# Kernel optimization log

Measured on AMD Instinct MI355X. Metric: run time of the kernel, lower is better.

The kernel has to match this reference:

```python
import jax, jax.numpy as jnp
import numpy as np

N, D, H, DH, E = 4096, 256, 4, 64, 131072  # nodes, embed dim, heads, head dim, edges
ALPHA = 0.2  # LeakyReLU negative slope
NEG = -9.0e15  # mask fill value from the torch code (-9000000000000000.0)


def setup_inputs() -> dict:
    key = jax.random.key(0)
    ks = jax.random.split(key, 10)
    x = jax.random.normal(ks[0], (N, D), dtype=jnp.float32)
    edge_index = jax.random.randint(ks[1], (2, E), 0, N, dtype=jnp.int32)
    edge_vals = jax.random.uniform(ks[2], (E,), dtype=jnp.float32)
    # EdgeWeightAttention MLP: Linear(2D -> D), ReLU, Linear(D -> 1)
    W1 = jax.random.normal(ks[3], (2 * D, D), dtype=jnp.float32) * (1.0 / np.sqrt(2 * D))
    b1 = jnp.zeros((D,), dtype=jnp.float32)
    W2 = jax.random.normal(ks[4], (D, 1), dtype=jnp.float32) * (1.0 / np.sqrt(D))
    b2 = jnp.zeros((1,), dtype=jnp.float32)
    # Per-head GAT params (stacked over heads): W [H, D, DH], a_src/a_dst [H, DH]
    gain = 1.414
    W = jax.random.normal(ks[5], (H, D, DH), dtype=jnp.float32) * (gain * np.sqrt(2.0 / (D + DH)))
    a_src = jax.random.normal(ks[6], (H, DH), dtype=jnp.float32) * (gain * np.sqrt(2.0 / (1 + DH)))
    a_dst = jax.random.normal(ks[7], (H, DH), dtype=jnp.float32) * (gain * np.sqrt(2.0 / (1 + DH)))
    return {"x": x, "edge_vals": edge_vals, "W1": W1, "b1": b1, "W2": W2, "b2": b2,
            "W": W, "a_src": a_src, "a_dst": a_dst, "edge_index": edge_index}


def reference(x, edge_vals, W1, b1, W2, b2, W, a_src, a_dst, edge_index):
    n = x.shape[0]
    row, col = edge_index[0], edge_index[1]
    # --- EdgeWeightAttention: gather endpoint features, tiny MLP + sigmoid, rescale edge values ---
    ef = jnp.concatenate([x[row], x[col]], axis=1)                       # [E, 2D]
    aw = jax.nn.sigmoid(jax.nn.relu(ef @ W1 + b1) @ W2 + b2)[:, 0]       # [E]
    new_vals = edge_vals * aw                                            # [E]
    # Densify reweighted sparse adj (values are positive -> used only as mask adj>0 in GAT)
    adj = jnp.zeros((n, n), dtype=x.dtype).at[row, col].set(new_vals)    # [N, N]
    # --- Multi-head GAT, vectorized over heads ---
    h = jnp.einsum('nd,hde->hne', x, W)                                  # [H, N, DH]
    esrc = jnp.einsum('hne,he->hn', h, a_src)                            # [H, N]
    edst = jnp.einsum('hne,he->hn', h, a_dst)                            # [H, N]
    e = jax.nn.leaky_relu(esrc[:, :, None] + edst[:, None, :], ALPHA)    # [H, N, N]
    e = jnp.where(adj[None, :, :] > 0, e, jnp.asarray(NEG, x.dtype))
    attn = jax.nn.softmax(e, axis=-1)                                    # [H, N, N]
    out = jnp.einsum('hij,hje->hie', attn, h)                            # [H, N, DH]
    return jnp.transpose(out, (1, 0, 2)).reshape(n, H * DH)              # [N, D]
```

## Files before the change

### kernel.cpp

```cpp
#include <hip/hip_runtime.h>
#include <hip/hip_bf16.h>

#define NN    4096
#define DD    256
#define HH    4
#define DHH   64
#define EDGES 131072
#define CAP   128
#define RPB   2
#define LRELU_ALPHA 0.2f

typedef __hip_bfloat16 bf16;
typedef __attribute__((ext_vector_type(8))) short short8v;
typedef __attribute__((ext_vector_type(4))) float f32x4;


__device__ __forceinline__ float bf_lo(unsigned int u) { return __uint_as_float(u << 16); }
__device__ __forceinline__ float bf_hi(unsigned int u) { return __uint_as_float(u & 0xffff0000u); }

__device__ __forceinline__ unsigned short f2bf_rne(float f) {
    unsigned int u = __float_as_uint(f);
    return (unsigned short)((u + 0x7fffu + ((u >> 16) & 1u)) >> 16);
}
__device__ __forceinline__ float bf2f(unsigned short s) {
    return __uint_as_float(((unsigned int)s) << 16);
}

__global__ __launch_bounds__(1024) void hproj_edges_kernel(
    const float* __restrict__ x, const float* __restrict__ W,
    const float* __restrict__ a_src, const float* __restrict__ a_dst,
    const int* __restrict__ ei, const float* __restrict__ ev,
    bf16* __restrict__ hb, float* __restrict__ esrc, float* __restrict__ edst,
    unsigned int* __restrict__ bmg)
{
    __shared__ unsigned short wlhi[2048 * 10];
    __shared__ unsigned short wllo[2048 * 10];
    __shared__ float pvs[16][16];
    __shared__ float pvd[16][16];

    const int t   = threadIdx.x;
    const int blk = blockIdx.x;
    const int h   = blk & 3;
    const int i0  = (blk >> 2) * 64;

    if (t < 512) {
        const int   e  = blk * 512 + t;
        const float vv = ev[e];
        const int   er = ei[e];
        const int   ec = ei[EDGES + e];
        if (vv > 0.f)
            atomicOr(&bmg[er * (NN / 32) + (ec >> 5)], 1u << (ec & 31));
    }

    {
        const float4* Ws = (const float4*)(W + (size_t)h * (DD * DHH));
        #pragma unroll
        for (int j = 0; j < 4; ++j) {
            const int fi = t + j * 1024;
            const float4 f = Ws[fi];
            const float v[4] = {f.x, f.y, f.z, f.w};
            #pragma unroll
            for (int c = 0; c < 4; ++c) {
                const int lin = fi * 4 + c;
                const int d = lin >> 6, dh = lin & 63;
                const int rec = (((dh >> 4) * 8 + (d >> 5)) << 6)
                              + ((d >> 3) & 3) * 16 + (dh & 15);
                const int off = rec * 10 + (d & 7);
                const unsigned short hi = f2bf_rne(v[c]);
                wlhi[off] = hi;
                wllo[off] = f2bf_rne(v[c] - bf2f(hi));
            }
        }
    }
    __syncthreads();

    const int wv   = t >> 6;
    const int m    = wv >> 2;
    const int q    = wv & 3;
    const int lane = t & 63;
    const int mrow = lane & 15;
    const int kgrp = lane >> 4;

    const float* xp = x + (size_t)(i0 + m * 16 + mrow) * DD + 8 * kgrp;
    const unsigned int* hi32 = (const unsigned int*)wlhi;
    const unsigned int* lo32 = (const unsigned int*)wllo;

    f32x4 acc = (f32x4){0.f, 0.f, 0.f, 0.f};

    #pragma unroll
    for (int ks = 0; ks < 8; ++ks) {
        const float4 u0 = *(const float4*)(xp + ks * 32);
        const float4 u1 = *(const float4*)(xp + ks * 32 + 4);
        const float v[8] = {u0.x, u0.y, u0.z, u0.w, u1.x, u1.y, u1.z, u1.w};
        short8v ah, al;
        #pragma unroll
        for (int e = 0; e < 8; ++e) {
            const unsigned short hi = f2bf_rne(v[e]);
            ah[e] = (short)hi;
            al[e] = (short)f2bf_rne(v[e] - bf2f(hi));
        }
        const int rb = ((q * 8 + ks) * 64 + lane) * 5;
        union { unsigned int u[4]; short8v s; } bh, bl;
        #pragma unroll
        for (int k = 0; k < 4; ++k) {
            bh.u[k] = hi32[rb + k];
            bl.u[k] = lo32[rb + k];
        }
        acc = __builtin_amdgcn_mfma_f32_16x16x32_bf16(ah, bh.s, acc, 0, 0, 0);
        acc = __builtin_amdgcn_mfma_f32_16x16x32_bf16(ah, bl.s, acc, 0, 0, 0);
        acc = __builtin_amdgcn_mfma_f32_16x16x32_bf16(al, bh.s, acc, 0, 0, 0);
    }

    {
        const int col = h * 64 + q * 16 + mrow;
        #pragma unroll
        for (int reg = 0; reg < 4; ++reg) {
            const int row = i0 + m * 16 + 4 * kgrp + reg;
            hb[(size_t)row * (HH * DHH) + col] = __float2bfloat16(acc[reg]);
        }
    }

    {
        const float as = a_src[h * DHH + q * 16 + mrow];
        const float ad = a_dst[h * DHH + q * 16 + mrow];
        float vs[4], vd[4];
        #pragma unroll
        for (int reg = 0; reg < 4; ++reg) {
            vs[reg] = acc[reg] * as;
            vd[reg] = acc[reg] * ad;
        }
        #pragma unroll
        for (int reg = 0; reg < 4; ++reg) {
            #pragma unroll
            for (int off = 1; off < 16; off <<= 1) {
                vs[reg] += __shfl_xor(vs[reg], off, 64);
                vd[reg] += __shfl_xor(vd[reg], off, 64);
            }
        }
        if (mrow == 0) {
            #pragma unroll
            for (int reg = 0; reg < 4; ++reg) {
                pvs[wv][4 * kgrp + reg] = vs[reg];
                pvd[wv][4 * kgrp + reg] = vd[reg];
            }
        }
    }
    __syncthreads();

    if (q == 0 && lane < 16) {
        float s = 0.f, d = 0.f;
        #pragma unroll
        for (int qq = 0; qq < 4; ++qq) {
            s += pvs[m * 4 + qq][lane];
            d += pvd[m * 4 + qq][lane];
        }
        const int row = i0 + m * 16 + lane;
        esrc[row * HH + h] = s;
        edst[row * HH + h] = d;
    }
}

__global__ __launch_bounds__(128) void attn_kernel(
    const unsigned int* __restrict__ bmg, const bf16* __restrict__ hb,
    const float* __restrict__ esrc, const float* __restrict__ edst,
    float* __restrict__ out)
{
    __shared__ int nbr[RPB][CAP];
    __shared__ __align__(16) float wts[RPB][CAP][HH];

    const int t = threadIdx.x;
    const int r = t >> 6, lane = t & 63;
    const int i = blockIdx.x * RPB + r;

    const uint2 wp = *(const uint2*)(bmg + (size_t)i * (NN / 32) + 2 * lane);
    const int c = __popc(wp.x) + __popc(wp.y);
    int inc = c;
    #pragma unroll
    for (int off = 1; off < 64; off <<= 1) {
        const int nn = __shfl_up(inc, off, 64);
        if (lane >= off) inc += nn;
    }
    int p = inc - c;
    const int deg = min(__shfl(inc, 63, 64), CAP);
    unsigned int w = wp.x;
    while (w) { const int b = __ffs(w) - 1; w &= w - 1; if (p < CAP) nbr[r][p] = (lane << 6) + b; ++p; }
    w = wp.y;
    while (w) { const int b = __ffs(w) - 1; w &= w - 1; if (p < CAP) nbr[r][p] = (lane << 6) + 32 + b; ++p; }
    __syncthreads();

    const int head = lane >> 4;
    float4 acc = make_float4(0.f, 0.f, 0.f, 0.f);
    float4 sm  = make_float4(0.f, 0.f, 0.f, 0.f);

    if (deg > 0) {
        const float4 es4 = *(const float4*)(esrc + (size_t)i * HH);
        float4 mx = make_float4(-INFINITY, -INFINITY, -INFINITY, -INFINITY);
        for (int k = lane; k < deg; k += 64) {
            const float4 ed = *(const float4*)(edst + (size_t)nbr[r][k] * HH);
            float4 e4;
            e4.x = es4.x + ed.x; e4.x = e4.x > 0.f ? e4.x : LRELU_ALPHA * e4.x;
            e4.y = es4.y + ed.y; e4.y = e4.y > 0.f ? e4.y : LRELU_ALPHA * e4.y;
            e4.z = es4.z + ed.z; e4.z = e4.z > 0.f ? e4.z : LRELU_ALPHA * e4.z;
            e4.w = es4.w + ed.w; e4.w = e4.w > 0.f ? e4.w : LRELU_ALPHA * e4.w;
            *(float4*)&wts[r][k][0] = e4;
            mx.x = fmaxf(mx.x, e4.x); mx.y = fmaxf(mx.y, e4.y);
            mx.z = fmaxf(mx.z, e4.z); mx.w = fmaxf(mx.w, e4.w);
        }
        #pragma unroll
        for (int off = 32; off; off >>= 1) {
            mx.x = fmaxf(mx.x, __shfl_xor(mx.x, off, 64));
            mx.y = fmaxf(mx.y, __shfl_xor(mx.y, off, 64));
            mx.z = fmaxf(mx.z, __shfl_xor(mx.z, off, 64));
            mx.w = fmaxf(mx.w, __shfl_xor(mx.w, off, 64));
        }
        for (int k = lane; k < deg; k += 64) {
            float4 e4 = *(const float4*)&wts[r][k][0];
            e4.x = expf(e4.x - mx.x); e4.y = expf(e4.y - mx.y);
            e4.z = expf(e4.z - mx.z); e4.w = expf(e4.w - mx.w);
            *(float4*)&wts[r][k][0] = e4;
            sm.x += e4.x; sm.y += e4.y; sm.z += e4.z; sm.w += e4.w;
        }
        #pragma unroll
        for (int off = 32; off; off >>= 1) {
            sm.x += __shfl_xor(sm.x, off, 64);
            sm.y += __shfl_xor(sm.y, off, 64);
            sm.z += __shfl_xor(sm.z, off, 64);
            sm.w += __shfl_xor(sm.w, off, 64);
        }
    }
    __syncthreads();

    float inv;
    if (deg == 0) {
        const uint2* hp = (const uint2*)hb + lane;
        for (int j = 0; j < NN; ++j) {
            const uint2 u = hp[(size_t)j * 64];
            acc.x += bf_lo(u.x); acc.y += bf_hi(u.x);
            acc.z += bf_lo(u.y); acc.w += bf_hi(u.y);
        }
        inv = 1.f / NN;
    } else {
        const uint2* hp = (const uint2*)hb;
        int k = 0;
        for (; k + 3 < deg; k += 4) {
            const int j0 = nbr[r][k],     j1 = nbr[r][k + 1];
            const int j2 = nbr[r][k + 2], j3 = nbr[r][k + 3];
            const uint2 u0 = hp[(size_t)j0 * 64 + lane];
            const uint2 u1 = hp[(size_t)j1 * 64 + lane];
            const uint2 u2 = hp[(size_t)j2 * 64 + lane];
            const uint2 u3 = hp[(size_t)j3 * 64 + lane];
            const float w0 = wts[r][k][head],     w1 = wts[r][k + 1][head];
            const float w2 = wts[r][k + 2][head], w3 = wts[r][k + 3][head];
            acc.x = fmaf(w0, bf_lo(u0.x), acc.x); acc.y = fmaf(w0, bf_hi(u0.x), acc.y);
            acc.z = fmaf(w0, bf_lo(u0.y), acc.z); acc.w = fmaf(w0, bf_hi(u0.y), acc.w);
            acc.x = fmaf(w1, bf_lo(u1.x), acc.x); acc.y = fmaf(w1, bf_hi(u1.x), acc.y);
            acc.z = fmaf(w1, bf_lo(u1.y), acc.z); acc.w = fmaf(w1, bf_hi(u1.y), acc.w);
            acc.x = fmaf(w2, bf_lo(u2.x), acc.x); acc.y = fmaf(w2, bf_hi(u2.x), acc.y);
            acc.z = fmaf(w2, bf_lo(u2.y), acc.z); acc.w = fmaf(w2, bf_hi(u2.y), acc.w);
            acc.x = fmaf(w3, bf_lo(u3.x), acc.x); acc.y = fmaf(w3, bf_hi(u3.x), acc.y);
            acc.z = fmaf(w3, bf_lo(u3.y), acc.z); acc.w = fmaf(w3, bf_hi(u3.y), acc.w);
        }
        for (; k < deg; ++k) {
            const uint2 u = hp[(size_t)nbr[r][k] * 64 + lane];
            const float wk = wts[r][k][head];
            acc.x = fmaf(wk, bf_lo(u.x), acc.x); acc.y = fmaf(wk, bf_hi(u.x), acc.y);
            acc.z = fmaf(wk, bf_lo(u.y), acc.z); acc.w = fmaf(wk, bf_hi(u.y), acc.w);
        }
        const float s = head == 0 ? sm.x : head == 1 ? sm.y : head == 2 ? sm.z : sm.w;
        inv = 1.f / s;
    }

    float4 o;
    o.x = acc.x * inv; o.y = acc.y * inv; o.z = acc.z * inv; o.w = acc.w * inv;
    *(float4*)(out + (size_t)i * (HH * DHH) + 4 * lane) = o;
}

extern "C" void kernel_launch(void* const* d_in, const int* in_sizes, int n_in,
                              void* d_out, int out_size, void* d_ws, size_t ws_size,
                              hipStream_t stream)
{
    const float* x     = (const float*)d_in[0];
    const float* ev    = (const float*)d_in[1];
    const float* W     = (const float*)d_in[6];
    const float* a_src = (const float*)d_in[7];
    const float* a_dst = (const float*)d_in[8];
    const int*   ei    = (const int*)d_in[9];
    float* out = (float*)d_out;

    char* ws = (char*)d_ws;
    bf16*  hb    = (bf16*)ws;
    float* esrc  = (float*)(ws + 2097152);
    float* edst  = (float*)(ws + 2162688);
    unsigned int* bmg = (unsigned int*)(ws + 2228224);

    hipMemsetAsync(bmg, 0, NN * (NN / 32) * sizeof(unsigned int), stream);
    hproj_edges_kernel<<<256, 1024, 0, stream>>>(x, W, a_src, a_dst, ei, ev,
                                                 hb, esrc, edst, bmg);
    attn_kernel<<<NN / RPB, 128, 0, stream>>>(bmg, hb, esrc, edst, out);
}
```

Measured before the change: 102.9 us.

## Fuse memset, projection and attention into one cooperative kernel with grid syncs

Replaces the memset plus two kernel launches with a single cooperative kernel of 256 blocks x 1024 threads. The blocks zero the adjacency bitmap themselves, do the projection and edge scatter, then run the attention phase with 16 rows per block, separated by grid-wide syncs. Shared memory is a union of the two phases' layouts. This removes launch overhead and inter-kernel gaps, but attention now runs on only 256 large blocks instead of 2048 small ones, and grid.sync adds its own cost.

```diff
diff --git a/kernel.cpp b/kernel.cpp
--- a/kernel.cpp
+++ b/kernel.cpp
@@ -1,5 +1,8 @@
 #include <hip/hip_runtime.h>
 #include <hip/hip_bf16.h>
+#include <hip/hip_cooperative_groups.h>
+
+namespace cg = cooperative_groups;
 
 #define NN    4096
 #define DD    256
@@ -7,7 +10,6 @@
 #define DHH   64
 #define EDGES 131072
 #define CAP   128
-#define RPB   2
 #define LRELU_ALPHA 0.2f
 
 typedef __hip_bfloat16 bf16;
@@ -26,253 +28,262 @@
     return __uint_as_float(((unsigned int)s) << 16);
 }
 
-__global__ __launch_bounds__(1024) void hproj_edges_kernel(
-    const float* __restrict__ x, const float* __restrict__ W,
-    const float* __restrict__ a_src, const float* __restrict__ a_dst,
-    const int* __restrict__ ei, const float* __restrict__ ev,
+struct Phase1LDS {
+    unsigned short wlhi[2048 * 10];
+    unsigned short wllo[2048 * 10];
+    float pvs[16][16];
+    float pvd[16][16];
+};
+struct Phase2LDS {
+    int   nbr[16][CAP];
+    float wts[16][CAP][HH];
+};
+union FusedLDS { Phase1LDS p1; Phase2LDS p2; };
+
+__global__ __launch_bounds__(1024, 4) void fused_kernel(
+    const float* __restrict__ x, const float* __restrict__ ev,
+    const float* __restrict__ W, const float* __restrict__ a_src,
+    const float* __restrict__ a_dst, const int* __restrict__ ei,
     bf16* __restrict__ hb, float* __restrict__ esrc, float* __restrict__ edst,
-    unsigned int* __restrict__ bmg)
+    unsigned int* __restrict__ bmg, float* __restrict__ out)
 {
-    __shared__ unsigned short wlhi[2048 * 10];
-    __shared__ unsigned short wllo[2048 * 10];
-    __shared__ float pvs[16][16];
-    __shared__ float pvd[16][16];
+    __shared__ FusedLDS sh;
+    cg::grid_group grid = cg::this_grid();
 
     const int t   = threadIdx.x;
     const int blk = blockIdx.x;
-    const int h   = blk & 3;
-    const int i0  = (blk >> 2) * 64;
-
-    if (t < 512) {
-        const int   e  = blk * 512 + t;
-        const float vv = ev[e];
-        const int   er = ei[e];
-        const int   ec = ei[EDGES + e];
-        if (vv > 0.f)
-            atomicOr(&bmg[er * (NN / 32) + (ec >> 5)], 1u << (ec & 31));
+
+    ((uint2*)bmg)[blk * 1024 + t] = make_uint2(0u, 0u);
+    grid.sync();
+
+    {
+        const int h  = blk & 3;
+        const int i0 = (blk >> 2) * 64;
+
+        if (t < 512) {
+            const int   e  = blk * 512 + t;
+            const float vv = ev[e];
+            const int   er = ei[e];
+            const int   ec = ei[EDGES + e];
+            if (vv > 0.f)
+                atomicOr(&bmg[er * (NN / 32) + (ec >> 5)], 1u << (ec & 31));
+        }
+
+        {
+            const float4* Ws = (const float4*)(W + (size_t)h * (DD * DHH));
+            #pragma unroll
+            for (int j = 0; j < 4; ++j) {
+                const int fi = t + j * 1024;
+                const float4 f = Ws[fi];
+                const float v[4] = {f.x, f.y, f.z, f.w};
+                #pragma unroll
+                for (int c = 0; c < 4; ++c) {
+                    const int lin = fi * 4 + c;
+                    const int d = lin >> 6, dh = lin & 63;
+                    const int rec = (((dh >> 4) * 8 + (d >> 5)) << 6)
+                                  + ((d >> 3) & 3) * 16 + (dh & 15);
+                    const int off = rec * 10 + (d & 7);
+                    const unsigned short hi = f2bf_rne(v[c]);
+                    sh.p1.wlhi[off] = hi;
+                    sh.p1.wllo[off] = f2bf_rne(v[c] - bf2f(hi));
+                }
+            }
+        }
+        __syncthreads();
+
+        const int wv   = t >> 6;
+        const int m    = wv >> 2;
+        const int q    = wv & 3;
+        const int lane = t & 63;
+        const int mrow = lane & 15;
+        const int kgrp = lane >> 4;
+
+        const float* xp = x + (size_t)(i0 + m * 16 + mrow) * DD + 8 * kgrp;
+        const unsigned int* hi32 = (const unsigned int*)sh.p1.wlhi;
+        const unsigned int* lo32 = (const unsigned int*)sh.p1.wllo;
+
+        f32x4 acc = (f32x4){0.f, 0.f, 0.f, 0.f};
+
+        #pragma unroll
+        for (int ks = 0; ks < 8; ++ks) {
+            const float4 u0 = *(const float4*)(xp + ks * 32);
+            const float4 u1 = *(const float4*)(xp + ks * 32 + 4);
+            const float v[8] = {u0.x, u0.y, u0.z, u0.w, u1.x, u1.y, u1.z, u1.w};
+            short8v ah, al;
+            #pragma unroll
+            for (int e = 0; e < 8; ++e) {
+                const unsigned short hi = f2bf_rne(v[e]);
+                ah[e] = (short)hi;
+                al[e] = (short)f2bf_rne(v[e] - bf2f(hi));
+            }
+            const int rb = ((q * 8 + ks) * 64 + lane) * 5;
+            union { unsigned int u[4]; short8v s; } bh, bl;
+            #pragma unroll
+            for (int k = 0; k < 4; ++k) {
+                bh.u[k] = hi32[rb + k];
+                bl.u[k] = lo32[rb + k];
+            }
+            acc = __builtin_amdgcn_mfma_f32_16x16x32_bf16(ah, bh.s, acc, 0, 0, 0);
+            acc = __builtin_amdgcn_mfma_f32_16x16x32_bf16(ah, bl.s, acc, 0, 0, 0);
+            acc = __builtin_amdgcn_mfma_f32_16x16x32_bf16(al, bh.s, acc, 0, 0, 0);
+        }
+
+        {
+            const int col = h * 64 + q * 16 + mrow;
+            #pragma unroll
+            for (int reg = 0; reg < 4; ++reg) {
+                const int row = i0 + m * 16 + 4 * kgrp + reg;
+                hb[(size_t)row * (HH * DHH) + col] = __float2bfloat16(acc[reg]);
+            }
+        }
+
+        {
+            const float as = a_src[h * DHH + q * 16 + mrow];
+            const float ad = a_dst[h * DHH + q * 16 + mrow];
+            float vs[4], vd[4];
+            #pragma unroll
+            for (int reg = 0; reg < 4; ++reg) {
+                vs[reg] = acc[reg] * as;
+                vd[reg] = acc[reg] * ad;
+            }
+            #pragma unroll
+            for (int reg = 0; reg < 4; ++reg) {
+                #pragma unroll
+                for (int off = 1; off < 16; off <<= 1) {
+                    vs[reg] += __shfl_xor(vs[reg], off, 64);
+                    vd[reg] += __shfl_xor(vd[reg], off, 64);
+                }
+            }
+            if (mrow == 0) {
+                #pragma unroll
+                for (int reg = 0; reg < 4; ++reg) {
+                    sh.p1.pvs[wv][4 * kgrp + reg] = vs[reg];
+                    sh.p1.pvd[wv][4 * kgrp + reg] = vd[reg];
+                }
+            }
+        }
+        __syncthreads();
+
+        if (q == 0 && lane < 16) {
+            float s = 0.f, d = 0.f;
+            #pragma unroll
+            for (int qq = 0; qq < 4; ++qq) {
+                s += sh.p1.pvs[m * 4 + qq][lane];
+                d += sh.p1.pvd[m * 4 + qq][lane];
+            }
+            const int row = i0 + m * 16 + lane;
+            esrc[row * HH + h] = s;
+            edst[row * HH + h] = d;
+        }
     }
+    grid.sync();
 
     {
-        const float4* Ws = (const float4*)(W + (size_t)h * (DD * DHH));
+        const int w = t >> 6, lane = t & 63;
+        const int i = blk * 16 + w;
+
+        const uint2 wp = *(const uint2*)(bmg + (size_t)i * (NN / 32) + 2 * lane);
+        const int c = __popc(wp.x) + __popc(wp.y);
+        int inc = c;
         #pragma unroll
-        for (int j = 0; j < 4; ++j) {
-            const int fi = t + j * 1024;
-            const float4 f = Ws[fi];
-            const float v[4] = {f.x, f.y, f.z, f.w};
-            #pragma unroll
-            for (int c = 0; c < 4; ++c) {
-                const int lin = fi * 4 + c;
-                const int d = lin >> 6, dh = lin & 63;
-                const int rec = (((dh >> 4) * 8 + (d >> 5)) << 6)
-                              + ((d >> 3) & 3) * 16 + (dh & 15);
-                const int off = rec * 10 + (d & 7);
-                const unsigned short hi = f2bf_rne(v[c]);
-                wlhi[off] = hi;
-                wllo[off] = f2bf_rne(v[c] - bf2f(hi));
-            }
-        }
+        for (int off = 1; off < 64; off <<= 1) {
+            const int nn = __shfl_up(inc, off, 64);
+            if (lane >= off) inc += nn;
+        }
+        int p = inc - c;
+        const int deg = min(__shfl(inc, 63, 64), CAP);
+        unsigned int bw = wp.x;
+        while (bw) { const int b = __ffs(bw) - 1; bw &= bw - 1; if (p < CAP) sh.p2.nbr[w][p] = (lane << 6) + b; ++p; }
+        bw = wp.y;
+        while (bw) { const int b = __ffs(bw) - 1; bw &= bw - 1; if (p < CAP) sh.p2.nbr[w][p] = (lane << 6) + 32 + b; ++p; }
+        __syncthreads();
+
+        const int head = lane >> 4;
+        float4 acc = make_float4(0.f, 0.f, 0.f, 0.f);
+        float4 sm  = make_float4(0.f, 0.f, 0.f, 0.f);
+
+        if (deg > 0) {
+            const float4 es4 = *(const float4*)(esrc + (size_t)i * HH);
+            float4 mx = make_float4(-INFINITY, -INFINITY, -INFINITY, -INFINITY);
+            for (int k = lane; k < deg; k += 64) {
+                const float4 ed = *(const float4*)(edst + (size_t)sh.p2.nbr[w][k] * HH);
+                float4 e4;
+                e4.x = es4.x + ed.x; e4.x = e4.x > 0.f ? e4.x : LRELU_ALPHA * e4.x;
+                e4.y = es4.y + ed.y; e4.y = e4.y > 0.f ? e4.y : LRELU_ALPHA * e4.y;
+                e4.z = es4.z + ed.z; e4.z = e4.z > 0.f ? e4.z : LRELU_ALPHA * e4.z;
+                e4.w = es4.w + ed.w; e4.w = e4.w > 0.f ? e4.w : LRELU_ALPHA * e4.w;
+                *(float4*)&sh.p2.wts[w][k][0] = e4;
+                mx.x = fmaxf(mx.x, e4.x); mx.y = fmaxf(mx.y, e4.y);
+                mx.z = fmaxf(mx.z, e4.z); mx.w = fmaxf(mx.w, e4.w);
+            }
+            #pragma unroll
+            for (int off = 32; off; off >>= 1) {
+                mx.x = fmaxf(mx.x, __shfl_xor(mx.x, off, 64));
+                mx.y = fmaxf(mx.y, __shfl_xor(mx.y, off, 64));
+                mx.z = fmaxf(mx.z, __shfl_xor(mx.z, off, 64));
+                mx.w = fmaxf(mx.w, __shfl_xor(mx.w, off, 64));
+            }
+            for (int k = lane; k < deg; k += 64) {
+                float4 e4 = *(const float4*)&sh.p2.wts[w][k][0];
+                e4.x = expf(e4.x - mx.x); e4.y = expf(e4.y - mx.y);
+                e4.z = expf(e4.z - mx.z); e4.w = expf(e4.w - mx.w);
+                *(float4*)&sh.p2.wts[w][k][0] = e4;
+                sm.x += e4.x; sm.y += e4.y; sm.z += e4.z; sm.w += e4.w;
+            }
+            #pragma unroll
+            for (int off = 32; off; off >>= 1) {
+                sm.x += __shfl_xor(sm.x, off, 64);
+                sm.y += __shfl_xor(sm.y, off, 64);
+                sm.z += __shfl_xor(sm.z, off, 64);
+                sm.w += __shfl_xor(sm.w, off, 64);
+            }
+        }
+        __syncthreads();
+
+        float inv;
+        if (deg == 0) {
+            const uint2* hp = (const uint2*)hb + lane;
+            for (int j = 0; j < NN; ++j) {
+                const uint2 u = hp[(size_t)j * 64];
+                acc.x += bf_lo(u.x); acc.y += bf_hi(u.x);
+                acc.z += bf_lo(u.y); acc.w += bf_hi(u.y);
+            }
+            inv = 1.f / NN;
+        } else {
+            const uint2* hp = (const uint2*)hb;
+            int k = 0;
+            for (; k + 3 < deg; k += 4) {
+                const int j0 = sh.p2.nbr[w][k],     j1 = sh.p2.nbr[w][k + 1];
+                const int j2 = sh.p2.nbr[w][k + 2], j3 = sh.p2.nbr[w][k + 3];
+                const uint2 u0 = hp[(size_t)j0 * 64 + lane];
+                const uint2 u1 = hp[(size_t)j1 * 64 + lane];
+                const uint2 u2 = hp[(size_t)j2 * 64 + lane];
+                const uint2 u3 = hp[(size_t)j3 * 64 + lane];
+                const float w0 = sh.p2.wts[w][k][head],     w1 = sh.p2.wts[w][k + 1][head];
+                const float w2 = sh.p2.wts[w][k + 2][head], w3 = sh.p2.wts[w][k + 3][head];
+                acc.x = fmaf(w0, bf_lo(u0.x), acc.x); acc.y = fmaf(w0, bf_hi(u0.x), acc.y);
+                acc.z = fmaf(w0, bf_lo(u0.y), acc.z); acc.w = fmaf(w0, bf_hi(u0.y), acc.w);
+                acc.x = fmaf(w1, bf_lo(u1.x), acc.x); acc.y = fmaf(w1, bf_hi(u1.x), acc.y);
+                acc.z = fmaf(w1, bf_lo(u1.y), acc.z); acc.w = fmaf(w1, bf_hi(u1.y), acc.w);
+                acc.x = fmaf(w2, bf_lo(u2.x), acc.x); acc.y = fmaf(w2, bf_hi(u2.x), acc.y);
+                acc.z = fmaf(w2, bf_lo(u2.y), acc.z); acc.w = fmaf(w2, bf_hi(u2.y), acc.w);
+                acc.x = fmaf(w3, bf_lo(u3.x), acc.x); acc.y = fmaf(w3, bf_hi(u3.x), acc.y);
+                acc.z = fmaf(w3, bf_lo(u3.y), acc.z); acc.w = fmaf(w3, bf_hi(u3.y), acc.w);
+            }
+            for (; k < deg; ++k) {
+                const uint2 u = hp[(size_t)sh.p2.nbr[w][k] * 64 + lane];
+                const float wk = sh.p2.wts[w][k][head];
+                acc.x = fmaf(wk, bf_lo(u.x), acc.x); acc.y = fmaf(wk, bf_hi(u.x), acc.y);
+                acc.z = fmaf(wk, bf_lo(u.y), acc.z); acc.w = fmaf(wk, bf_hi(u.y), acc.w);
+            }
+            const float s = head == 0 ? sm.x : head == 1 ? sm.y : head == 2 ? sm.z : sm.w;
+            inv = 1.f / s;
+        }
+
+        float4 o;
+        o.x = acc.x * inv; o.y = acc.y * inv; o.z = acc.z * inv; o.w = acc.w * inv;
+        *(float4*)(out + (size_t)i * (HH * DHH) + 4 * lane) = o;
     }
-    __syncthreads();
-
-    const int wv   = t >> 6;
-    const int m    = wv >> 2;
-    const int q    = wv & 3;
-    const int lane = t & 63;
-    const int mrow = lane & 15;
-    const int kgrp = lane >> 4;
-
-    const float* xp = x + (size_t)(i0 + m * 16 + mrow) * DD + 8 * kgrp;
-    const unsigned int* hi32 = (const unsigned int*)wlhi;
-    const unsigned int* lo32 = (const unsigned int*)wllo;
-
-    f32x4 acc = (f32x4){0.f, 0.f, 0.f, 0.f};
-
-    #pragma unroll
-    for (int ks = 0; ks < 8; ++ks) {
-        const float4 u0 = *(const float4*)(xp + ks * 32);
-        const float4 u1 = *(const float4*)(xp + ks * 32 + 4);
-        const float v[8] = {u0.x, u0.y, u0.z, u0.w, u1.x, u1.y, u1.z, u1.w};
-        short8v ah, al;
-        #pragma unroll
-        for (int e = 0; e < 8; ++e) {
-            const unsigned short hi = f2bf_rne(v[e]);
-            ah[e] = (short)hi;
-            al[e] = (short)f2bf_rne(v[e] - bf2f(hi));
-        }
-        const int rb = ((q * 8 + ks) * 64 + lane) * 5;
-        union { unsigned int u[4]; short8v s; } bh, bl;
-        #pragma unroll
-        for (int k = 0; k < 4; ++k) {
-            bh.u[k] = hi32[rb + k];
-            bl.u[k] = lo32[rb + k];
-        }
-        acc = __builtin_amdgcn_mfma_f32_16x16x32_bf16(ah, bh.s, acc, 0, 0, 0);
-        acc = __builtin_amdgcn_mfma_f32_16x16x32_bf16(ah, bl.s, acc, 0, 0, 0);
-        acc = __builtin_amdgcn_mfma_f32_16x16x32_bf16(al, bh.s, acc, 0, 0, 0);
-    }
-
-    {
-        const int col = h * 64 + q * 16 + mrow;
-        #pragma unroll
-        for (int reg = 0; reg < 4; ++reg) {
-            const int row = i0 + m * 16 + 4 * kgrp + reg;
-            hb[(size_t)row * (HH * DHH) + col] = __float2bfloat16(acc[reg]);
-        }
-    }
-
-    {
-        const float as = a_src[h * DHH + q * 16 + mrow];
-        const float ad = a_dst[h * DHH + q * 16 + mrow];
-        float vs[4], vd[4];
-        #pragma unroll
-        for (int reg = 0; reg < 4; ++reg) {
-            vs[reg] = acc[reg] * as;
-            vd[reg] = acc[reg] * ad;
-        }
-        #pragma unroll
-        for (int reg = 0; reg < 4; ++reg) {
-            #pragma unroll
-            for (int off = 1; off < 16; off <<= 1) {
-                vs[reg] += __shfl_xor(vs[reg], off, 64);
-                vd[reg] += __shfl_xor(vd[reg], off, 64);
-            }
-        }
-        if (mrow == 0) {
-            #pragma unroll
-            for (int reg = 0; reg < 4; ++reg) {
-                pvs[wv][4 * kgrp + reg] = vs[reg];
-                pvd[wv][4 * kgrp + reg] = vd[reg];
-            }
-        }
-    }
-    __syncthreads();
-
-    if (q == 0 && lane < 16) {
-        float s = 0.f, d = 0.f;
-        #pragma unroll
-        for (int qq = 0; qq < 4; ++qq) {
-            s += pvs[m * 4 + qq][lane];
-            d += pvd[m * 4 + qq][lane];
-        }
-        const int row = i0 + m * 16 + lane;
-        esrc[row * HH + h] = s;
-        edst[row * HH + h] = d;
-    }
-}
-
-__global__ __launch_bounds__(128) void attn_kernel(
-    const unsigned int* __restrict__ bmg, const bf16* __restrict__ hb,
-    const float* __restrict__ esrc, const float* __restrict__ edst,
-    float* __restrict__ out)
-{
-    __shared__ int nbr[RPB][CAP];
-    __shared__ __align__(16) float wts[RPB][CAP][HH];
-
-    const int t = threadIdx.x;
-    const int r = t >> 6, lane = t & 63;
-    const int i = blockIdx.x * RPB + r;
-
-    const uint2 wp = *(const uint2*)(bmg + (size_t)i * (NN / 32) + 2 * lane);
-    const int c = __popc(wp.x) + __popc(wp.y);
-    int inc = c;
-    #pragma unroll
-    for (int off = 1; off < 64; off <<= 1) {
-        const int nn = __shfl_up(inc, off, 64);
-        if (lane >= off) inc += nn;
-    }
-    int p = inc - c;
-    const int deg = min(__shfl(inc, 63, 64), CAP);
-    unsigned int w = wp.x;
-    while (w) { const int b = __ffs(w) - 1; w &= w - 1; if (p < CAP) nbr[r][p] = (lane << 6) + b; ++p; }
-    w = wp.y;
-    while (w) { const int b = __ffs(w) - 1; w &= w - 1; if (p < CAP) nbr[r][p] = (lane << 6) + 32 + b; ++p; }
-    __syncthreads();
-
-    const int head = lane >> 4;
-    float4 acc = make_float4(0.f, 0.f, 0.f, 0.f);
-    float4 sm  = make_float4(0.f, 0.f, 0.f, 0.f);
-
-    if (deg > 0) {
-        const float4 es4 = *(const float4*)(esrc + (size_t)i * HH);
-        float4 mx = make_float4(-INFINITY, -INFINITY, -INFINITY, -INFINITY);
-        for (int k = lane; k < deg; k += 64) {
-            const float4 ed = *(const float4*)(edst + (size_t)nbr[r][k] * HH);
-            float4 e4;
-            e4.x = es4.x + ed.x; e4.x = e4.x > 0.f ? e4.x : LRELU_ALPHA * e4.x;
-            e4.y = es4.y + ed.y; e4.y = e4.y > 0.f ? e4.y : LRELU_ALPHA * e4.y;
-            e4.z = es4.z + ed.z; e4.z = e4.z > 0.f ? e4.z : LRELU_ALPHA * e4.z;
-            e4.w = es4.w + ed.w; e4.w = e4.w > 0.f ? e4.w : LRELU_ALPHA * e4.w;
-            *(float4*)&wts[r][k][0] = e4;
-            mx.x = fmaxf(mx.x, e4.x); mx.y = fmaxf(mx.y, e4.y);
-            mx.z = fmaxf(mx.z, e4.z); mx.w = fmaxf(mx.w, e4.w);
-        }
-        #pragma unroll
-        for (int off = 32; off; off >>= 1) {
-            mx.x = fmaxf(mx.x, __shfl_xor(mx.x, off, 64));
-            mx.y = fmaxf(mx.y, __shfl_xor(mx.y, off, 64));
-            mx.z = fmaxf(mx.z, __shfl_xor(mx.z, off, 64));
-            mx.w = fmaxf(mx.w, __shfl_xor(mx.w, off, 64));
-        }
-        for (int k = lane; k < deg; k += 64) {
-            float4 e4 = *(const float4*)&wts[r][k][0];
-            e4.x = expf(e4.x - mx.x); e4.y = expf(e4.y - mx.y);
-            e4.z = expf(e4.z - mx.z); e4.w = expf(e4.w - mx.w);
-            *(float4*)&wts[r][k][0] = e4;
-            sm.x += e4.x; sm.y += e4.y; sm.z += e4.z; sm.w += e4.w;
-        }
-        #pragma unroll
-        for (int off = 32; off; off >>= 1) {
-            sm.x += __shfl_xor(sm.x, off, 64);
-            sm.y += __shfl_xor(sm.y, off, 64);
-            sm.z += __shfl_xor(sm.z, off, 64);
-            sm.w += __shfl_xor(sm.w, off, 64);
-        }
-    }
-    __syncthreads();
-
-    float inv;
-    if (deg == 0) {
-        const uint2* hp = (const uint2*)hb + lane;
-        for (int j = 0; j < NN; ++j) {
-            const uint2 u = hp[(size_t)j * 64];
-            acc.x += bf_lo(u.x); acc.y += bf_hi(u.x);
-            acc.z += bf_lo(u.y); acc.w += bf_hi(u.y);
-        }
-        inv = 1.f / NN;
-    } else {
-        const uint2* hp = (const uint2*)hb;
-        int k = 0;
-        for (; k + 3 < deg; k += 4) {
-            const int j0 = nbr[r][k],     j1 = nbr[r][k + 1];
-            const int j2 = nbr[r][k + 2], j3 = nbr[r][k + 3];
-            const uint2 u0 = hp[(size_t)j0 * 64 + lane];
-            const uint2 u1 = hp[(size_t)j1 * 64 + lane];
-            const uint2 u2 = hp[(size_t)j2 * 64 + lane];
-            const uint2 u3 = hp[(size_t)j3 * 64 + lane];
-            const float w0 = wts[r][k][head],     w1 = wts[r][k + 1][head];
-            const float w2 = wts[r][k + 2][head], w3 = wts[r][k + 3][head];
-            acc.x = fmaf(w0, bf_lo(u0.x), acc.x); acc.y = fmaf(w0, bf_hi(u0.x), acc.y);
-            acc.z = fmaf(w0, bf_lo(u0.y), acc.z); acc.w = fmaf(w0, bf_hi(u0.y), acc.w);
-            acc.x = fmaf(w1, bf_lo(u1.x), acc.x); acc.y = fmaf(w1, bf_hi(u1.x), acc.y);
-            acc.z = fmaf(w1, bf_lo(u1.y), acc.z); acc.w = fmaf(w1, bf_hi(u1.y), acc.w);
-            acc.x = fmaf(w2, bf_lo(u2.x), acc.x); acc.y = fmaf(w2, bf_hi(u2.x), acc.y);
-            acc.z = fmaf(w2, bf_lo(u2.y), acc.z); acc.w = fmaf(w2, bf_hi(u2.y), acc.w);
-            acc.x = fmaf(w3, bf_lo(u3.x), acc.x); acc.y = fmaf(w3, bf_hi(u3.x), acc.y);
-            acc.z = fmaf(w3, bf_lo(u3.y), acc.z); acc.w = fmaf(w3, bf_hi(u3.y), acc.w);
-        }
-        for (; k < deg; ++k) {
-            const uint2 u = hp[(size_t)nbr[r][k] * 64 + lane];
-            const float wk = wts[r][k][head];
-            acc.x = fmaf(wk, bf_lo(u.x), acc.x); acc.y = fmaf(wk, bf_hi(u.x), acc.y);
-            acc.z = fmaf(wk, bf_lo(u.y), acc.z); acc.w = fmaf(wk, bf_hi(u.y), acc.w);
-        }
-        const float s = head == 0 ? sm.x : head == 1 ? sm.y : head == 2 ? sm.z : sm.w;
-        inv = 1.f / s;
-    }
-
-    float4 o;
-    o.x = acc.x * inv; o.y = acc.y * inv; o.z = acc.z * inv; o.w = acc.w * inv;
-    *(float4*)(out + (size_t)i * (HH * DHH) + 4 * lane) = o;
 }
 
 extern "C" void kernel_launch(void* const* d_in, const int* in_sizes, int n_in,
@@ -293,8 +304,9 @@
     float* edst  = (float*)(ws + 2162688);
     unsigned int* bmg = (unsigned int*)(ws + 2228224);
 
-    hipMemsetAsync(bmg, 0, NN * (NN / 32) * sizeof(unsigned int), stream);
-    hproj_edges_kernel<<<256, 1024, 0, stream>>>(x, W, a_src, a_dst, ei, ev,
-                                                 hb, esrc, edst, bmg);
-    attn_kernel<<<NN / RPB, 128, 0, stream>>>(bmg, hb, esrc, edst, out);
+    void* args[] = {(void*)&x, (void*)&ev, (void*)&W, (void*)&a_src,
+                    (void*)&a_dst, (void*)&ei, (void*)&hb, (void*)&esrc,
+                    (void*)&edst, (void*)&bmg, (void*)&out};
+    hipLaunchCooperativeKernel((const void*)fused_kernel, dim3(256), dim3(1024),
+                               args, 0, stream);
 }
```

New measurement: 176.8 us. 1.72x slower.
